# Kernel optimization log

Measured on AMD Instinct MI355X. Metric: run time of the kernel, lower is better.

Reference implementation:

```python
import jax, jax.numpy as jnp
import numpy as np

N_NODES = 50000
N_EDGES = 800000
IN_DIM = 128
OUT_DIM = 128


def setup_inputs() -> dict:
    key = jax.random.key(0)
    k1, k2, k3, k4, k5, k6 = jax.random.split(key, 6)
    X = jax.random.normal(k1, (N_NODES, IN_DIM), dtype=jnp.float32)
    src = jax.random.randint(k2, (N_EDGES,), 0, N_NODES, dtype=jnp.int32)
    dst = jax.random.randint(k3, (N_EDGES,), 0, N_NODES, dtype=jnp.int32)
    # nn.Linear(in, out, bias=False) weight has shape (out, in)
    lim = 1.0 / np.sqrt(IN_DIM)
    W_self = jax.random.uniform(k4, (OUT_DIM, IN_DIM), dtype=jnp.float32, minval=-lim, maxval=lim)
    W_neigh = jax.random.uniform(k5, (OUT_DIM, IN_DIM), dtype=jnp.float32, minval=-lim, maxval=lim)
    bias = jnp.zeros((OUT_DIM,), dtype=jnp.float32)
    return {"X": X, "src": src, "dst": dst, "W_self": W_self, "W_neigh": W_neigh, "bias": bias}


def reference(X, src, dst, W_self, W_neigh, bias):
    # h_u = ReLU( W_self x_u + sum_{(v->u) in E} W_neigh x_v + bias )
    # Transform once per node (n_nodes x in_dim x out_dim GEMMs), then
    # gather transformed source features and scatter-add into destinations.
    h_self = jnp.einsum('ni,oi->no', X, W_self)        # [N, out]
    xw_neigh = jnp.einsum('ni,oi->no', X, W_neigh)     # [N, out]
    h_neigh = jax.ops.segment_sum(xw_neigh[src], dst, num_segments=N_NODES)
    return jax.nn.relu(h_self + h_neigh + bias)
```

## Files before the change

### kernel.cpp

```cpp
#include <hip/hip_runtime.h>

#define IN_DIM 128
#define OUT_DIM 128
#define BM 64
#define KT 32

__global__ void scatter_kernel(const float* __restrict__ X,
                               const int* __restrict__ src,
                               const int* __restrict__ dst,
                               float* __restrict__ A,
                               int n_edges) {
    int gtid = blockIdx.x * blockDim.x + threadIdx.x;
    int e = gtid >> 5;
    if (e >= n_edges) return;
    int sub = gtid & 31;
    int s = src[e];
    int d = dst[e];
    const float4 v = *reinterpret_cast<const float4*>(
        X + (size_t)s * IN_DIM + sub * 4);
    float* o = A + (size_t)d * IN_DIM + sub * 4;
    unsafeAtomicAdd(o + 0, v.x);
    unsafeAtomicAdd(o + 1, v.y);
    unsafeAtomicAdd(o + 2, v.z);
    unsafeAtomicAdd(o + 3, v.w);
}

__global__ void hist_kernel(const int* __restrict__ dst, int* __restrict__ counts,
                            int n_edges) {
    int e = blockIdx.x * blockDim.x + threadIdx.x;
    if (e < n_edges) atomicAdd(&counts[dst[e]], 1);
}

__global__ __launch_bounds__(256)
void scan1_kernel(const int* __restrict__ counts, int* __restrict__ offs,
                  int* __restrict__ bsums, int n) {
    __shared__ int tmp[256];
    const int tid = threadIdx.x;
    const int i = blockIdx.x * 256 + tid;
    const int v = (i < n) ? counts[i] : 0;
    tmp[tid] = v;
    __syncthreads();
    #pragma unroll
    for (int d = 1; d < 256; d <<= 1) {
        int t = (tid >= d) ? tmp[tid - d] : 0;
        __syncthreads();
        tmp[tid] += t;
        __syncthreads();
    }
    if (i < n) offs[i] = tmp[tid] - v;
    if (tid == 255) bsums[blockIdx.x] = tmp[255];
}

__global__ __launch_bounds__(256)
void scan2_kernel(int* __restrict__ bsums, int nb) {
    __shared__ int tmp[256];
    __shared__ int carry;
    const int tid = threadIdx.x;
    if (tid == 0) carry = 0;
    __syncthreads();
    for (int base = 0; base < nb; base += 256) {
        const int i = base + tid;
        const int v = (i < nb) ? bsums[i] : 0;
        tmp[tid] = v;
        __syncthreads();
        #pragma unroll
        for (int d = 1; d < 256; d <<= 1) {
            int t = (tid >= d) ? tmp[tid - d] : 0;
            __syncthreads();
            tmp[tid] += t;
            __syncthreads();
        }
        if (i < nb) bsums[i] = carry + tmp[tid] - v;
        __syncthreads();
        if (tid == 0) carry += tmp[255];
        __syncthreads();
    }
}

__global__ __launch_bounds__(256)
void scan3_kernel(int* __restrict__ offs, const int* __restrict__ bsums,
                  int* __restrict__ cursor, int n) {
    const int i = blockIdx.x * 256 + threadIdx.x;
    if (i < n) {
        const int o = offs[i] + bsums[blockIdx.x];
        offs[i] = o;
        cursor[i] = o;
    }
}

__global__ void bucket_kernel(const int* __restrict__ src,
                              const int* __restrict__ dst,
                              int* __restrict__ cursor,
                              int* __restrict__ src_sorted, int n_edges) {
    int e = blockIdx.x * blockDim.x + threadIdx.x;
    if (e < n_edges) {
        const int pos = atomicAdd(&cursor[dst[e]], 1);
        src_sorted[pos] = src[e];
    }
}

__global__ __launch_bounds__(256)
void accum_kernel(const float* __restrict__ X,
                  const int* __restrict__ offs,
                  const int* __restrict__ src_sorted,
                  float* __restrict__ A, int n_nodes, int n_edges) {
    const int tid = threadIdx.x;
    const int u = blockIdx.x * 8 + (tid >> 5);
    if (u >= n_nodes) return;
    const int sub = tid & 31;

    const int beg = offs[u];
    const int end = (u == n_nodes - 1) ? n_edges : offs[u + 1];

    float4 acc = make_float4(0.f, 0.f, 0.f, 0.f);
    for (int e = beg; e < end; ++e) {
        const int s = src_sorted[e];
        const float4 v = *reinterpret_cast<const float4*>(
            X + (size_t)s * IN_DIM + sub * 4);
        acc.x += v.x; acc.y += v.y; acc.z += v.z; acc.w += v.w;
    }
    *reinterpret_cast<float4*>(A + (size_t)u * IN_DIM + sub * 4) = acc;
}

__global__ __launch_bounds__(256)
void gemm_kernel(const float* __restrict__ X,
                 const float* __restrict__ A,
                 const float* __restrict__ Wself,
                 const float* __restrict__ Wneigh,
                 const float* __restrict__ bias,
                 float* __restrict__ out,
                 int n_nodes) {
    __shared__ alignas(16) float Wt[KT][132];
    __shared__ alignas(16) float Xs[BM][KT + 4];

    const int tid   = threadIdx.x;
    const int o_grp = tid & 31;
    const int n_grp = tid >> 5;
    const int node0 = blockIdx.x * BM;

    float acc[8][4];
    #pragma unroll
    for (int i = 0; i < 8; ++i)
        #pragma unroll
        for (int j = 0; j < 4; ++j) acc[i][j] = 0.f;

    for (int kt = 0; kt < 2 * IN_DIM; kt += KT) {
        const float* Wsrc = (kt < IN_DIM) ? Wself : Wneigh;
        const float* Fsrc = (kt < IN_DIM) ? X : A;
        const int kbase = kt & (IN_DIM - 1);

        __syncthreads();

        {
            const int k4 = tid & 7;
            int o = tid >> 3;
            #pragma unroll
            for (int p = 0; p < 4; ++p, o += 32) {
                float4 w = *reinterpret_cast<const float4*>(
                    Wsrc + o * IN_DIM + kbase + k4 * 4);
                Wt[k4 * 4 + 0][o] = w.x;
                Wt[k4 * 4 + 1][o] = w.y;
                Wt[k4 * 4 + 2][o] = w.z;
                Wt[k4 * 4 + 3][o] = w.w;
            }
        }
        {
            const int k4 = tid & 7;
            int n = tid >> 3;
            #pragma unroll
            for (int p = 0; p < 2; ++p, n += 32) {
                const int node = node0 + n;
                float4 x = make_float4(0.f, 0.f, 0.f, 0.f);
                if (node < n_nodes)
                    x = *reinterpret_cast<const float4*>(
                        Fsrc + (size_t)node * IN_DIM + kbase + k4 * 4);
                *reinterpret_cast<float4*>(&Xs[n][k4 * 4]) = x;
            }
        }
        __syncthreads();

        #pragma unroll
        for (int k4 = 0; k4 < KT; k4 += 4) {
            float4 w0 = *reinterpret_cast<const float4*>(&Wt[k4 + 0][o_grp * 4]);
            float4 w1 = *reinterpret_cast<const float4*>(&Wt[k4 + 1][o_grp * 4]);
            float4 w2 = *reinterpret_cast<const float4*>(&Wt[k4 + 2][o_grp * 4]);
            float4 w3 = *reinterpret_cast<const float4*>(&Wt[k4 + 3][o_grp * 4]);
            #pragma unroll
            for (int nn = 0; nn < 8; ++nn) {
                float4 x = *reinterpret_cast<const float4*>(
                    &Xs[n_grp * 8 + nn][k4]);
                acc[nn][0] = fmaf(x.x, w0.x, acc[nn][0]);
                acc[nn][0] = fmaf(x.y, w1.x, acc[nn][0]);
                acc[nn][0] = fmaf(x.z, w2.x, acc[nn][0]);
                acc[nn][0] = fmaf(x.w, w3.x, acc[nn][0]);
                acc[nn][1] = fmaf(x.x, w0.y, acc[nn][1]);
                acc[nn][1] = fmaf(x.y, w1.y, acc[nn][1]);
                acc[nn][1] = fmaf(x.z, w2.y, acc[nn][1]);
                acc[nn][1] = fmaf(x.w, w3.y, acc[nn][1]);
                acc[nn][2] = fmaf(x.x, w0.z, acc[nn][2]);
                acc[nn][2] = fmaf(x.y, w1.z, acc[nn][2]);
                acc[nn][2] = fmaf(x.z, w2.z, acc[nn][2]);
                acc[nn][2] = fmaf(x.w, w3.z, acc[nn][2]);
                acc[nn][3] = fmaf(x.x, w0.w, acc[nn][3]);
                acc[nn][3] = fmaf(x.y, w1.w, acc[nn][3]);
                acc[nn][3] = fmaf(x.z, w2.w, acc[nn][3]);
                acc[nn][3] = fmaf(x.w, w3.w, acc[nn][3]);
            }
        }
    }

    const float4 b = *reinterpret_cast<const float4*>(bias + o_grp * 4);
    #pragma unroll
    for (int nn = 0; nn < 8; ++nn) {
        const int node = node0 + n_grp * 8 + nn;
        if (node < n_nodes) {
            float4 r;
            r.x = fmaxf(acc[nn][0] + b.x, 0.f);
            r.y = fmaxf(acc[nn][1] + b.y, 0.f);
            r.z = fmaxf(acc[nn][2] + b.z, 0.f);
            r.w = fmaxf(acc[nn][3] + b.w, 0.f);
            *reinterpret_cast<float4*>(
                out + (size_t)node * OUT_DIM + o_grp * 4) = r;
        }
    }
}

extern "C" void kernel_launch(void* const* d_in, const int* in_sizes, int n_in,
                              void* d_out, int out_size, void* d_ws, size_t ws_size,
                              hipStream_t stream) {
    const float* X      = (const float*)d_in[0];
    const int*   src    = (const int*)d_in[1];
    const int*   dst    = (const int*)d_in[2];
    const float* Wself  = (const float*)d_in[3];
    const float* Wneigh = (const float*)d_in[4];
    const float* bias   = (const float*)d_in[5];
    float*       out    = (float*)d_out;

    const int n_nodes = in_sizes[0] / IN_DIM;
    const int n_edges = in_sizes[1];
    const int nb = (n_nodes + 255) / 256;

    char* w = (char*)d_ws;
    auto take = [&](size_t bytes) {
        char* p = w;
        w += (bytes + 15) & ~(size_t)15;
        return p;
    };
    float* A         = (float*)take((size_t)n_nodes * IN_DIM * sizeof(float));
    int*   counts    = (int*)take((size_t)n_nodes * sizeof(int));
    int*   offs      = (int*)take((size_t)n_nodes * sizeof(int));
    int*   cursor    = (int*)take((size_t)n_nodes * sizeof(int));
    int*   bsums     = (int*)take((size_t)nb * sizeof(int));
    int*   srcsorted = (int*)take((size_t)n_edges * sizeof(int));
    const size_t needed = (size_t)(w - (char*)d_ws);

    const int eblocks = (n_edges + 255) / 256;

    if (needed <= ws_size) {
        hipMemsetAsync(counts, 0, (size_t)n_nodes * sizeof(int), stream);
        hist_kernel<<<eblocks, 256, 0, stream>>>(dst, counts, n_edges);
        scan1_kernel<<<nb, 256, 0, stream>>>(counts, offs, bsums, n_nodes);
        scan2_kernel<<<1, 256, 0, stream>>>(bsums, nb);
        scan3_kernel<<<nb, 256, 0, stream>>>(offs, bsums, cursor, n_nodes);
        bucket_kernel<<<eblocks, 256, 0, stream>>>(src, dst, cursor, srcsorted,
                                                   n_edges);
        accum_kernel<<<(n_nodes + 7) / 8, 256, 0, stream>>>(
            X, offs, srcsorted, A, n_nodes, n_edges);
    } else {
        hipMemsetAsync(A, 0, (size_t)n_nodes * IN_DIM * sizeof(float), stream);
        const long long sthreads = (long long)n_edges * 32;
        const int sblocks = (int)((sthreads + 255) / 256);
        scatter_kernel<<<sblocks, 256, 0, stream>>>(X, src, dst, A, n_edges);
    }

    const int gblocks = (n_nodes + BM - 1) / BM;
    gemm_kernel<<<gblocks, 256, 0, stream>>>(X, A, Wself, Wneigh, bias, out,
                                             n_nodes);
}
```

Measured before the change: 296.0 us.

## Use split-bf16 MFMA GEMM with vectorized histogram and unrolled gather

Replaces the fp32 FMA GEMM with an MFMA bf16 GEMM. Features and weights are each split into hi and lo bf16 parts, and three products (hi*hi, lo*hi, hi*lo) per segment approximate fp32 accuracy. The accumulation kernel now writes A directly as hi/lo bf16 halves with a 4-way unrolled gather, and the histogram reads dst as int4. This adds split kernels and stages the split X in the output buffer. The cost is extra memory traffic and a small precision loss compared with true fp32.

Measured after the change: 264.4 us. 10.7% less time.

```diff
diff --git a/kernel.cpp b/kernel.cpp
--- a/kernel.cpp
+++ b/kernel.cpp
@@ -4,6 +4,17 @@
 #define OUT_DIM 128
 #define BM 64
 #define KT 32
+
+typedef __attribute__((ext_vector_type(8))) short short8v;
+typedef __attribute__((ext_vector_type(4))) float float4v;
+
+__device__ __forceinline__ unsigned short bf16_hi(float x) {
+    unsigned int u = __float_as_uint(x);
+    return (unsigned short)((u + 0x7fffu + ((u >> 16) & 1u)) >> 16);
+}
+__device__ __forceinline__ float bf16_tof(unsigned short h) {
+    return __uint_as_float(((unsigned int)h) << 16);
+}
 
 __global__ void scatter_kernel(const float* __restrict__ X,
                                const int* __restrict__ src,
@@ -27,8 +38,17 @@
 
 __global__ void hist_kernel(const int* __restrict__ dst, int* __restrict__ counts,
                             int n_edges) {
-    int e = blockIdx.x * blockDim.x + threadIdx.x;
-    if (e < n_edges) atomicAdd(&counts[dst[e]], 1);
+    int i = blockIdx.x * blockDim.x + threadIdx.x;
+    int e0 = i * 4;
+    if (e0 + 4 <= n_edges) {
+        int4 d4 = *reinterpret_cast<const int4*>(dst + e0);
+        atomicAdd(&counts[d4.x], 1);
+        atomicAdd(&counts[d4.y], 1);
+        atomicAdd(&counts[d4.z], 1);
+        atomicAdd(&counts[d4.w], 1);
+    } else {
+        for (int e = e0; e < n_edges; ++e) atomicAdd(&counts[dst[e]], 1);
+    }
 }
 
 __global__ __launch_bounds__(256)
@@ -100,10 +120,12 @@
 }
 
 __global__ __launch_bounds__(256)
-void accum_kernel(const float* __restrict__ X,
-                  const int* __restrict__ offs,
-                  const int* __restrict__ src_sorted,
-                  float* __restrict__ A, int n_nodes, int n_edges) {
+void accum_split_kernel(const float* __restrict__ X,
+                        const int* __restrict__ offs,
+                        const int* __restrict__ src_sorted,
+                        unsigned short* __restrict__ Ahi,
+                        unsigned short* __restrict__ Alo,
+                        int n_nodes, int n_edges) {
     const int tid = threadIdx.x;
     const int u = blockIdx.x * 8 + (tid >> 5);
     if (u >= n_nodes) return;
@@ -113,13 +135,196 @@
     const int end = (u == n_nodes - 1) ? n_edges : offs[u + 1];
 
     float4 acc = make_float4(0.f, 0.f, 0.f, 0.f);
-    for (int e = beg; e < end; ++e) {
+    int e = beg;
+    for (; e + 4 <= end; e += 4) {
+        const int s0 = src_sorted[e + 0];
+        const int s1 = src_sorted[e + 1];
+        const int s2 = src_sorted[e + 2];
+        const int s3 = src_sorted[e + 3];
+        const float4 v0 = *reinterpret_cast<const float4*>(X + (size_t)s0 * IN_DIM + sub * 4);
+        const float4 v1 = *reinterpret_cast<const float4*>(X + (size_t)s1 * IN_DIM + sub * 4);
+        const float4 v2 = *reinterpret_cast<const float4*>(X + (size_t)s2 * IN_DIM + sub * 4);
+        const float4 v3 = *reinterpret_cast<const float4*>(X + (size_t)s3 * IN_DIM + sub * 4);
+        acc.x += v0.x + v1.x + v2.x + v3.x;
+        acc.y += v0.y + v1.y + v2.y + v3.y;
+        acc.z += v0.z + v1.z + v2.z + v3.z;
+        acc.w += v0.w + v1.w + v2.w + v3.w;
+    }
+    for (; e < end; ++e) {
         const int s = src_sorted[e];
-        const float4 v = *reinterpret_cast<const float4*>(
-            X + (size_t)s * IN_DIM + sub * 4);
+        const float4 v = *reinterpret_cast<const float4*>(X + (size_t)s * IN_DIM + sub * 4);
         acc.x += v.x; acc.y += v.y; acc.z += v.z; acc.w += v.w;
     }
-    *reinterpret_cast<float4*>(A + (size_t)u * IN_DIM + sub * 4) = acc;
+
+    ushort4 hi, lo;
+    hi.x = bf16_hi(acc.x); lo.x = bf16_hi(acc.x - bf16_tof(hi.x));
+    hi.y = bf16_hi(acc.y); lo.y = bf16_hi(acc.y - bf16_tof(hi.y));
+    hi.z = bf16_hi(acc.z); lo.z = bf16_hi(acc.z - bf16_tof(hi.z));
+    hi.w = bf16_hi(acc.w); lo.w = bf16_hi(acc.w - bf16_tof(hi.w));
+    *reinterpret_cast<ushort4*>(Ahi + (size_t)u * IN_DIM + sub * 4) = hi;
+    *reinterpret_cast<ushort4*>(Alo + (size_t)u * IN_DIM + sub * 4) = lo;
+}
+
+__global__ void xsplit_kernel(const float* __restrict__ X,
+                              unsigned short* __restrict__ Xsp, int n_nodes) {
+    int i = blockIdx.x * blockDim.x + threadIdx.x;
+    if (i >= n_nodes * 32) return;
+    const int node = i >> 5, g = i & 31;
+    const float4 x = *reinterpret_cast<const float4*>(X + (size_t)node * IN_DIM + g * 4);
+    ushort4 hi, lo;
+    hi.x = bf16_hi(x.x); lo.x = bf16_hi(x.x - bf16_tof(hi.x));
+    hi.y = bf16_hi(x.y); lo.y = bf16_hi(x.y - bf16_tof(hi.y));
+    hi.z = bf16_hi(x.z); lo.z = bf16_hi(x.z - bf16_tof(hi.z));
+    hi.w = bf16_hi(x.w); lo.w = bf16_hi(x.w - bf16_tof(hi.w));
+    *reinterpret_cast<ushort4*>(Xsp + (size_t)node * 256 + g * 4) = hi;
+    *reinterpret_cast<ushort4*>(Xsp + (size_t)node * 256 + 128 + g * 4) = lo;
+}
+
+__global__ void wsplit_kernel(const float* __restrict__ W1,
+                              const float* __restrict__ W2,
+                              unsigned short* __restrict__ W1h,
+                              unsigned short* __restrict__ W1l,
+                              unsigned short* __restrict__ W2h,
+                              unsigned short* __restrict__ W2l) {
+    int i = blockIdx.x * blockDim.x + threadIdx.x;
+    if (i >= OUT_DIM * IN_DIM) return;
+    float a = W1[i], b = W2[i];
+    unsigned short ah = bf16_hi(a), bh = bf16_hi(b);
+    W1h[i] = ah; W1l[i] = bf16_hi(a - bf16_tof(ah));
+    W2h[i] = bh; W2l[i] = bf16_hi(b - bf16_tof(bh));
+}
+
+__global__ __launch_bounds__(256, 4)
+void mfma_gemm_kernel(const unsigned short* Xsp,
+                      const unsigned short* __restrict__ Ahi,
+                      const unsigned short* __restrict__ Alo,
+                      const unsigned short* __restrict__ W1h,
+                      const unsigned short* __restrict__ W1l,
+                      const unsigned short* __restrict__ W2h,
+                      const unsigned short* __restrict__ W2l,
+                      const float* __restrict__ bias,
+                      float* out,
+                      int n_nodes) {
+    __shared__ unsigned short Fs[64 * 64];
+    __shared__ unsigned short Ws[128 * 64];
+
+    const int tid  = threadIdx.x;
+    const int lane = tid & 63;
+    const int wid  = tid >> 6;
+    const int wm   = wid >> 1;
+    const int wn   = wid & 1;
+    const int lr   = lane & 15;
+    const int lk   = lane >> 4;
+    const int node0 = blockIdx.x * 64;
+
+    const int fr = tid >> 3;
+    const int c  = tid & 7;
+    const int swz = (c ^ (fr & 7)) * 8;
+
+    float4v acc[2][4];
+    #pragma unroll
+    for (int mi = 0; mi < 2; ++mi)
+        #pragma unroll
+        for (int ni = 0; ni < 4; ++ni) acc[mi][ni] = (float4v)0.f;
+
+    const unsigned short* wseg[6] = {W1h, W1l, W1h, W2h, W2l, W2h};
+
+    short8v fv[2], wv[4];
+
+    {
+        const int seg = 0, khalf = 0;
+        #pragma unroll
+        for (int j = 0; j < 2; ++j) {
+            const int node = node0 + fr + j * 32;
+            short8v v = (short8v)0;
+            if (node < n_nodes)
+                v = *reinterpret_cast<const short8v*>(
+                    Xsp + (size_t)node * 256 + khalf + c * 8);
+            fv[j] = v;
+        }
+        #pragma unroll
+        for (int j = 0; j < 4; ++j)
+            wv[j] = *reinterpret_cast<const short8v*>(
+                wseg[seg] + (size_t)(fr + j * 32) * 128 + khalf + c * 8);
+    }
+
+    #pragma unroll
+    for (int t = 0; t < 12; ++t) {
+        __syncthreads();
+        #pragma unroll
+        for (int j = 0; j < 2; ++j)
+            *reinterpret_cast<short8v*>(&Fs[(fr + j * 32) * 64 + swz]) = fv[j];
+        #pragma unroll
+        for (int j = 0; j < 4; ++j)
+            *reinterpret_cast<short8v*>(&Ws[(fr + j * 32) * 64 + swz]) = wv[j];
+        __syncthreads();
+
+        if (t < 11) {
+            const int tn = t + 1;
+            const int seg = tn >> 1;
+            const int khalf = (tn & 1) * 64;
+            #pragma unroll
+            for (int j = 0; j < 2; ++j) {
+                const int node = node0 + fr + j * 32;
+                short8v v = (short8v)0;
+                if (node < n_nodes) {
+                    if (seg < 3) {
+                        v = *reinterpret_cast<const short8v*>(
+                            Xsp + (size_t)node * 256 + (seg == 2 ? 128 : 0) +
+                            khalf + c * 8);
+                    } else {
+                        const unsigned short* Ap = (seg == 5) ? Alo : Ahi;
+                        v = *reinterpret_cast<const short8v*>(
+                            Ap + (size_t)node * 128 + khalf + c * 8);
+                    }
+                }
+                fv[j] = v;
+            }
+            #pragma unroll
+            for (int j = 0; j < 4; ++j)
+                wv[j] = *reinterpret_cast<const short8v*>(
+                    wseg[seg] + (size_t)(fr + j * 32) * 128 + khalf + c * 8);
+        }
+
+        #pragma unroll
+        for (int ks = 0; ks < 2; ++ks) {
+            const int cc = ((ks * 4 + lk) ^ (lr & 7)) * 8;
+            short8v a[2], b[4];
+            #pragma unroll
+            for (int mi = 0; mi < 2; ++mi) {
+                const int row = wm * 32 + mi * 16 + lr;
+                a[mi] = *reinterpret_cast<const short8v*>(&Fs[row * 64 + cc]);
+            }
+            #pragma unroll
+            for (int ni = 0; ni < 4; ++ni) {
+                const int o = wn * 64 + ni * 16 + lr;
+                b[ni] = *reinterpret_cast<const short8v*>(&Ws[o * 64 + cc]);
+            }
+            #pragma unroll
+            for (int mi = 0; mi < 2; ++mi)
+                #pragma unroll
+                for (int ni = 0; ni < 4; ++ni)
+                    acc[mi][ni] = __builtin_amdgcn_mfma_f32_16x16x32_bf16(
+                        a[mi], b[ni], acc[mi][ni], 0, 0, 0);
+        }
+    }
+
+    #pragma unroll
+    for (int ni = 0; ni < 4; ++ni) {
+        const int o = wn * 64 + ni * 16 + lr;
+        const float bo = bias[o];
+        #pragma unroll
+        for (int mi = 0; mi < 2; ++mi) {
+            const int nodeb = node0 + wm * 32 + mi * 16 + lk * 4;
+            #pragma unroll
+            for (int r = 0; r < 4; ++r) {
+                const int node = nodeb + r;
+                if (node < n_nodes)
+                    out[(size_t)node * OUT_DIM + o] =
+                        fmaxf(acc[mi][ni][r] + bo, 0.f);
+            }
+        }
+    }
 }
 
 __global__ __launch_bounds__(256)
@@ -148,9 +353,7 @@
         const float* Wsrc = (kt < IN_DIM) ? Wself : Wneigh;
         const float* Fsrc = (kt < IN_DIM) ? X : A;
         const int kbase = kt & (IN_DIM - 1);
-
-        __syncthreads();
-
+        __syncthreads();
         {
             const int k4 = tid & 7;
             int o = tid >> 3;
@@ -178,7 +381,6 @@
             }
         }
         __syncthreads();
-
         #pragma unroll
         for (int k4 = 0; k4 < KT; k4 += 4) {
             float4 w0 = *reinterpret_cast<const float4*>(&Wt[k4 + 0][o_grp * 4]);
@@ -246,34 +448,44 @@
         w += (bytes + 15) & ~(size_t)15;
         return p;
     };
-    float* A         = (float*)take((size_t)n_nodes * IN_DIM * sizeof(float));
-    int*   counts    = (int*)take((size_t)n_nodes * sizeof(int));
-    int*   offs      = (int*)take((size_t)n_nodes * sizeof(int));
-    int*   cursor    = (int*)take((size_t)n_nodes * sizeof(int));
-    int*   bsums     = (int*)take((size_t)nb * sizeof(int));
-    int*   srcsorted = (int*)take((size_t)n_edges * sizeof(int));
+    unsigned short* Ahi = (unsigned short*)take((size_t)n_nodes * IN_DIM * 2);
+    unsigned short* Alo = (unsigned short*)take((size_t)n_nodes * IN_DIM * 2);
+    int* counts    = (int*)take((size_t)n_nodes * sizeof(int));
+    int* offs      = (int*)take((size_t)n_nodes * sizeof(int));
+    int* cursor    = (int*)take((size_t)n_nodes * sizeof(int));
+    int* bsums     = (int*)take((size_t)nb * sizeof(int));
+    int* srcsorted = (int*)take((size_t)n_edges * sizeof(int));
+    unsigned short* W1h = (unsigned short*)take((size_t)OUT_DIM * IN_DIM * 2);
+    unsigned short* W1l = (unsigned short*)take((size_t)OUT_DIM * IN_DIM * 2);
+    unsigned short* W2h = (unsigned short*)take((size_t)OUT_DIM * IN_DIM * 2);
+    unsigned short* W2l = (unsigned short*)take((size_t)OUT_DIM * IN_DIM * 2);
     const size_t needed = (size_t)(w - (char*)d_ws);
 
     const int eblocks = (n_edges + 255) / 256;
 
     if (needed <= ws_size) {
         hipMemsetAsync(counts, 0, (size_t)n_nodes * sizeof(int), stream);
-        hist_kernel<<<eblocks, 256, 0, stream>>>(dst, counts, n_edges);
+        hist_kernel<<<(n_edges / 4 + 256) / 256 + 1, 256, 0, stream>>>(dst, counts, n_edges);
         scan1_kernel<<<nb, 256, 0, stream>>>(counts, offs, bsums, n_nodes);
         scan2_kernel<<<1, 256, 0, stream>>>(bsums, nb);
         scan3_kernel<<<nb, 256, 0, stream>>>(offs, bsums, cursor, n_nodes);
         bucket_kernel<<<eblocks, 256, 0, stream>>>(src, dst, cursor, srcsorted,
                                                    n_edges);
-        accum_kernel<<<(n_nodes + 7) / 8, 256, 0, stream>>>(
-            X, offs, srcsorted, A, n_nodes, n_edges);
+        unsigned short* Xsp = (unsigned short*)d_out;
+        xsplit_kernel<<<(n_nodes * 32 + 255) / 256, 256, 0, stream>>>(X, Xsp, n_nodes);
+        wsplit_kernel<<<(OUT_DIM * IN_DIM + 255) / 256, 256, 0, stream>>>(
+            Wself, Wneigh, W1h, W1l, W2h, W2l);
+        accum_split_kernel<<<(n_nodes + 7) / 8, 256, 0, stream>>>(
+            X, offs, srcsorted, Ahi, Alo, n_nodes, n_edges);
+        mfma_gemm_kernel<<<(n_nodes + 63) / 64, 256, 0, stream>>>(
+            Xsp, Ahi, Alo, W1h, W1l, W2h, W2l, bias, out, n_nodes);
     } else {
+        float* A = (float*)d_ws;
         hipMemsetAsync(A, 0, (size_t)n_nodes * IN_DIM * sizeof(float), stream);
         const long long sthreads = (long long)n_edges * 32;
         const int sblocks = (int)((sthreads + 255) / 256);
         scatter_kernel<<<sblocks, 256, 0, stream>>>(X, src, dst, A, n_edges);
-    }
-
-    const int gblocks = (n_nodes + BM - 1) / BM;
-    gemm_kernel<<<gblocks, 256, 0, stream>>>(X, A, Wself, Wneigh, bias, out,
-                                             n_nodes);
-}
+        gemm_kernel<<<(n_nodes + BM - 1) / BM, 256, 0, stream>>>(
+            X, A, Wself, Wneigh, bias, out, n_nodes);
+    }
+}
```
